# Kernel tuning notes

Measured on AMD Instinct MI355X. Metric: run time of the kernel, lower is better.

The kernel has to match this reference:

```python
import jax, jax.numpy as jnp
import numpy as np

H = 4096      # hidden_size
D = 1024      # mem_dim
A = 512       # attn_dim
B, LQ, TM = 4, 2048, 1500
EPS = 1e-5


def _layernorm(x, w, b):
    mu = jnp.mean(x, axis=-1, keepdims=True)
    var = jnp.var(x, axis=-1, keepdims=True)
    return (x - mu) * jax.lax.rsqrt(var + EPS) * w + b


def setup_inputs() -> dict:
    key = jax.random.key(0)
    ks = jax.random.split(key, 12)
    s = lambda fan_in: 1.0 / np.sqrt(fan_in)
    return {
        "hidden": jax.random.normal(ks[0], (B, LQ, H), jnp.float32),
        "mem": jax.random.normal(ks[1], (B, TM, D), jnp.float32),
        "mem_mask": jnp.zeros((B, TM), dtype=bool),
        "Wq": jax.random.uniform(ks[2], (H, A), jnp.float32, -s(H), s(H)),
        "bq": jnp.zeros((A,), jnp.float32),
        "Wk": jax.random.uniform(ks[3], (D, A), jnp.float32, -s(D), s(D)),
        "bk": jnp.zeros((A,), jnp.float32),
        "Wv": jax.random.uniform(ks[4], (D, A), jnp.float32, -s(D), s(D)),
        "bv": jnp.zeros((A,), jnp.float32),
        "Wo": jax.random.uniform(ks[5], (A, H), jnp.float32, -s(A), s(A)),
        "bo": jnp.zeros((H,), jnp.float32),
        "ln_in_w": jnp.ones((H,), jnp.float32),
        "ln_in_b": jnp.zeros((H,), jnp.float32),
        "ln_out_w": jnp.ones((H,), jnp.float32),
        "ln_out_b": jnp.zeros((H,), jnp.float32),
        "gate_logit": jnp.float32(-2.0),
    }


def reference(hidden, mem, mem_mask, Wq, bq, Wk, bk, Wv, bv, Wo, bo,
              ln_in_w, ln_in_b, ln_out_w, ln_out_b, gate_logit):
    h_norm = _layernorm(hidden, ln_in_w, ln_in_b)            # [B,LQ,H]
    Q = h_norm @ Wq + bq                                     # [B,LQ,A]
    K = mem @ Wk + bk                                        # [B,TM,A]
    V = mem @ Wv + bv                                        # [B,TM,A]
    scale = 1.0 / jnp.sqrt(jnp.float32(Q.shape[-1]))
    scores = jnp.einsum('bqa,bka->bqk', Q, K) * scale        # [B,LQ,TM]
    scores = jnp.where(mem_mask[:, None, :], jnp.float32(-1e30), scores)
    attn = jax.nn.softmax(scores, axis=-1)
    context = jnp.einsum('bqk,bka->bqa', attn, V)            # [B,LQ,A]
    context_h = context @ Wo + bo                            # [B,LQ,H]
    out_base = _layernorm(hidden + context_h, ln_out_w, ln_out_b)
    g = jax.nn.sigmoid(gate_logit)
    return hidden + g * (out_base - hidden)
```

## Files before the change

### kernel.cpp

```cpp
#include <hip/hip_runtime.h>
#include <cstdint>
#include <cstddef>

#define H_   4096
#define D_   1024
#define A_   512
#define B_   4
#define LQ_  2048
#define TM_  1500
#define TMP_ 1536
#define EPS_ 1e-5f

typedef __attribute__((ext_vector_type(8))) _Float16 half8;
typedef __attribute__((ext_vector_type(4))) _Float16 half4v;
typedef __attribute__((ext_vector_type(4))) float f32x4;

__device__ __forceinline__ void gload_lds16(void* g, void* l) {
  __builtin_amdgcn_global_load_lds((__attribute__((address_space(1))) void*)g,
                                   (__attribute__((address_space(3))) void*)l,
                                   16, 0, 0);
}

template <int OUTMODE>
__device__ __forceinline__ void gemm_tile(
    const _Float16* __restrict__ A, int lda,
    const _Float16* __restrict__ Bt, int ldb,
    const float* __restrict__ bias,
    void* __restrict__ C, int ldc,
    int Mvalid, int m0, int n0, int kbase, int kiters, float scale,
    _Float16* As, _Float16* Bs,
    const unsigned char* __restrict__ mrow, float* __restrict__ lsum, int nvalid) {
  const int tid = threadIdx.x;
  const int lane = tid & 63;
  const int wave = tid >> 6;

  f32x4 acc[4][4];
#pragma unroll
  for (int i = 0; i < 4; ++i)
#pragma unroll
    for (int jj = 0; jj < 4; ++jj) acc[i][jj] = (f32x4){0.f, 0.f, 0.f, 0.f};

  const _Float16* gA[2];
  const _Float16* gB[2];
  _Float16* lA[2];
  _Float16* lB[2];
#pragma unroll
  for (int i = 0; i < 2; ++i) {
    const int c = wave * 64 + lane + 256 * i;
    const int r = c >> 2;
    const int cs = c & 3;
    const int col = (cs ^ ((r >> 1) & 3)) * 8;
    int ra = m0 + r;
    if (ra >= Mvalid) ra = Mvalid - 1;
    gA[i] = A + (size_t)ra * lda + kbase + col;
    gB[i] = Bt + (size_t)(n0 + r) * ldb + kbase + col;
    lA[i] = As + wave * 512 + i * 2048;
    lB[i] = Bs + wave * 512 + i * 2048;
  }

  const int wm = (wave >> 1) * 64;
  const int wn = (wave & 1) * 64;
  const int rsub = lane & 15;
  const int j = lane >> 4;
  const int slot = j ^ ((rsub >> 1) & 3);

  for (int kt = 0; kt < kiters; ++kt) {
    const int ko = kt * 32;
#pragma unroll
    for (int i = 0; i < 2; ++i) {
      gload_lds16((void*)(gA[i] + ko), (void*)lA[i]);
      gload_lds16((void*)(gB[i] + ko), (void*)lB[i]);
    }
    __syncthreads();
    half8 af[4], bfr[4];
#pragma unroll
    for (int x = 0; x < 4; ++x) {
      af[x]  = *(const half8*)&As[(wm + x * 16 + rsub) * 32 + slot * 8];
      bfr[x] = *(const half8*)&Bs[(wn + x * 16 + rsub) * 32 + slot * 8];
    }
#pragma unroll
    for (int mi = 0; mi < 4; ++mi)
#pragma unroll
      for (int ni = 0; ni < 4; ++ni)
        acc[mi][ni] = __builtin_amdgcn_mfma_f32_16x16x32_f16(af[mi], bfr[ni], acc[mi][ni], 0, 0, 0);
    __syncthreads();
  }

  const int cn = n0 + wn + rsub;
  const int rm = m0 + wm + j * 4;

  if (OUTMODE == 3) {
    bool ok[4];
#pragma unroll
    for (int ni = 0; ni < 4; ++ni) {
      const int n = cn + ni * 16;
      const int nc = n < nvalid ? n : nvalid - 1;
      ok[ni] = (n < nvalid) && (mrow[nc] == 0);
    }
#pragma unroll
    for (int mi = 0; mi < 4; ++mi) {
#pragma unroll
      for (int r = 0; r < 4; ++r) {
        const int m = rm + mi * 16 + r;
        float rowsum = 0.f;
#pragma unroll
        for (int ni = 0; ni < 4; ++ni) {
          const int n = cn + ni * 16;
          const float e = ok[ni] ? __expf(acc[mi][ni][r] * scale) : 0.f;
          ((_Float16*)C)[(size_t)m * ldc + n] = (_Float16)e;
          rowsum += e;
        }
#pragma unroll
        for (int d = 1; d < 16; d <<= 1) rowsum += __shfl_xor(rowsum, d);
        if (rsub == 0) atomicAdd(&lsum[m], rowsum);
      }
    }
    return;
  }

  if (OUTMODE == 1) {
#pragma unroll
    for (int ni = 0; ni < 4; ++ni) {
      const int n = cn + ni * 16;
      const float bi = bias ? bias[n] : 0.f;
#pragma unroll
      for (int mi = 0; mi < 4; ++mi) {
        half4v pk;
#pragma unroll
        for (int r = 0; r < 4; ++r) pk[r] = (_Float16)(acc[mi][ni][r] * scale + bi);
        *(half4v*)&((_Float16*)C)[(size_t)n * ldc + rm + mi * 16] = pk;
      }
    }
    return;
  }

#pragma unroll
  for (int ni = 0; ni < 4; ++ni) {
    const int n = cn + ni * 16;
    const float bi = (OUTMODE == 0 && bias) ? bias[n] : 0.f;
#pragma unroll
    for (int mi = 0; mi < 4; ++mi) {
#pragma unroll
      for (int r = 0; r < 4; ++r) {
        const int m = rm + mi * 16 + r;
        const float v = acc[mi][ni][r] * scale + bi;
        if (OUTMODE == 0) ((_Float16*)C)[(size_t)m * ldc + n] = (_Float16)v;
        else ((float*)C)[(size_t)m * ldc + n] = v;
      }
    }
  }
}

template <int OUTMODE>
__global__ __launch_bounds__(256) void gemm_nt_kernel(
    const _Float16* __restrict__ Aall, size_t strideA, int lda,
    const _Float16* __restrict__ Btall, size_t strideB, int ldb,
    const float* __restrict__ bias,
    void* __restrict__ Call, size_t strideC, size_t strideS,
    int ldc, int Mvalid, int kiters, int nslices, int sliceK, float scale) {
  __shared__ __align__(16) _Float16 As[4096];
  __shared__ __align__(16) _Float16 Bs[4096];
  const int z = blockIdx.z;
  const int batch = z / nslices;
  const int slice = z % nslices;
  const _Float16* A = Aall + (size_t)batch * strideA;
  const _Float16* Bt = Btall + (size_t)batch * strideB;
  char* C = (char*)Call + ((size_t)batch * strideC + (size_t)slice * strideS) *
                          (OUTMODE == 2 ? 4 : 2);
  gemm_tile<OUTMODE>(A, lda, Bt, ldb, bias, (void*)C, ldc, Mvalid,
                     blockIdx.y * 128, blockIdx.x * 128, slice * sliceK, kiters,
                     scale, As, Bs, nullptr, nullptr, 0);
}

__global__ __launch_bounds__(256) void scores_kernel(
    const _Float16* __restrict__ Qh, const _Float16* __restrict__ Kp,
    _Float16* __restrict__ sc, const unsigned char* __restrict__ mask,
    float* __restrict__ lsum) {
  __shared__ __align__(16) _Float16 As[4096];
  __shared__ __align__(16) _Float16 Bs[4096];
  const int b = blockIdx.z;
  gemm_tile<3>(Qh + (size_t)b * LQ_ * A_, A_, Kp + (size_t)b * TMP_ * A_, A_, nullptr,
               (void*)(sc + (size_t)b * LQ_ * TMP_), TMP_, LQ_,
               blockIdx.y * 128, blockIdx.x * 128, 0, 16, 0.044194173824159216f,
               As, Bs, mask + (size_t)b * TM_, lsum + (size_t)b * LQ_, TM_);
}

__global__ __launch_bounds__(256) void qkv_kernel(
    const _Float16* __restrict__ hnorm, const _Float16* __restrict__ WqT,
    float* __restrict__ Qpart,
    const _Float16* __restrict__ memh, const _Float16* __restrict__ WkT,
    const float* __restrict__ bk, _Float16* __restrict__ Kp,
    const _Float16* __restrict__ WvT, const float* __restrict__ bv,
    _Float16* __restrict__ VT) {
  __shared__ __align__(16) _Float16 As[4096];
  __shared__ __align__(16) _Float16 Bs[4096];
  const int bid = blockIdx.x;
  if (bid < 512) {
    const int nb = bid & 3, mb = (bid >> 2) & 63, ks = bid >> 8;
    gemm_tile<2>(hnorm, H_, WqT, H_, nullptr,
                 (void*)(Qpart + (size_t)ks * 8192 * A_), A_,
                 8192, mb * 128, nb * 128, ks * 2048, 64, 1.f, As, Bs,
                 nullptr, nullptr, 0);
  } else if (bid < 704) {
    const int t = bid - 512;
    const int nb = t & 3, mb = (t >> 2) % 12, b = t / 48;
    gemm_tile<0>(memh + (size_t)b * TM_ * D_, D_, WkT, D_, bk,
                 (void*)(Kp + (size_t)b * TMP_ * A_), A_,
                 TM_, mb * 128, nb * 128, 0, 32, 1.f, As, Bs,
                 nullptr, nullptr, 0);
  } else {
    const int t = bid - 704;
    const int nb = t & 3, mb = (t >> 2) % 12, b = t / 48;
    gemm_tile<1>(memh + (size_t)b * TM_ * D_, D_, WvT, D_, bv,
                 (void*)(VT + (size_t)b * A_ * TMP_), TMP_,
                 TM_, mb * 128, nb * 128, 0, 32, 1.f, As, Bs,
                 nullptr, nullptr, 0);
  }
}

__global__ __launch_bounds__(256) void qreduce_kernel(
    const float* __restrict__ p, const float* __restrict__ bias,
    _Float16* __restrict__ out, float* __restrict__ lsum) {
  const int bid = blockIdx.x;
  if (bid >= 4096) {
    lsum[(bid - 4096) * 256 + threadIdx.x] = 0.f;
    return;
  }
  const size_t i = ((size_t)bid * 256 + threadIdx.x) * 4;
  const float4 a = *(const float4*)(p + i);
  const float4 b = *(const float4*)(p + (size_t)8192 * A_ + i);
  const float4 bi = *(const float4*)(bias + (i & (A_ - 1)));
  half4v o;
  o.x = (_Float16)(a.x + b.x + bi.x);
  o.y = (_Float16)(a.y + b.y + bi.y);
  o.z = (_Float16)(a.z + b.z + bi.z);
  o.w = (_Float16)(a.w + b.w + bi.w);
  *(half4v*)(out + i) = o;
}

__global__ __launch_bounds__(256) void areduce_kernel(
    const float* __restrict__ p, const float* __restrict__ lsum,
    _Float16* __restrict__ out) {
  const size_t S = (size_t)B_ * LQ_ * A_;
  const size_t i = ((size_t)blockIdx.x * 256 + threadIdx.x) * 4;
  const float4 a = *(const float4*)(p + i);
  const float4 b = *(const float4*)(p + S + i);
  const float4 c = *(const float4*)(p + 2 * S + i);
  const float inv = 1.f / lsum[i >> 9];
  half4v o;
  o.x = (_Float16)((a.x + b.x + c.x) * inv);
  o.y = (_Float16)((a.y + b.y + c.y) * inv);
  o.z = (_Float16)((a.z + b.z + c.z) * inv);
  o.w = (_Float16)((a.w + b.w + c.w) * inv);
  *(half4v*)(out + i) = o;
}

__global__ __launch_bounds__(256) void prep_kernel(
    const float* __restrict__ hidden, const float* __restrict__ lnw,
    const float* __restrict__ lnb, _Float16* __restrict__ hnorm,
    const float* __restrict__ mem, _Float16* __restrict__ memh,
    const float* __restrict__ Wq, _Float16* __restrict__ WqT,
    const float* __restrict__ Wk, _Float16* __restrict__ WkT,
    const float* __restrict__ Wv, _Float16* __restrict__ WvT,
    const float* __restrict__ Wo, _Float16* __restrict__ WoT) {
  __shared__ float smem[32 * 33];
  int bid = blockIdx.x;
  const int t = threadIdx.x;
  if (bid < 8192) {
    const float* x = hidden + (size_t)bid * H_;
    _Float16* y = hnorm + (size_t)bid * H_;
    float4 v[4];
    float s = 0.f, ss = 0.f;
#pragma unroll
    for (int i = 0; i < 4; ++i) {
      v[i] = ((const float4*)x)[t + 256 * i];
      s  += v[i].x + v[i].y + v[i].z + v[i].w;
      ss += v[i].x * v[i].x + v[i].y * v[i].y + v[i].z * v[i].z + v[i].w * v[i].w;
    }
    const int lane = t & 63, wv = t >> 6;
#pragma unroll
    for (int off = 32; off; off >>= 1) { s += __shfl_down(s, off); ss += __shfl_down(ss, off); }
    if (lane == 0) { smem[wv] = s; smem[4 + wv] = ss; }
    __syncthreads();
    s  = smem[0] + smem[1] + smem[2] + smem[3];
    ss = smem[4] + smem[5] + smem[6] + smem[7];
    const float mu = s * (1.f / H_);
    const float var = ss * (1.f / H_) - mu * mu;
    const float rstd = rsqrtf(var + EPS_);
#pragma unroll
    for (int i = 0; i < 4; ++i) {
      float4 wv4 = ((const float4*)lnw)[t + 256 * i];
      float4 bv4 = ((const float4*)lnb)[t + 256 * i];
      half4v o;
      o.x = (_Float16)((v[i].x - mu) * rstd * wv4.x + bv4.x);
      o.y = (_Float16)((v[i].y - mu) * rstd * wv4.y + bv4.y);
      o.z = (_Float16)((v[i].z - mu) * rstd * wv4.z + bv4.z);
      o.w = (_Float16)((v[i].w - mu) * rstd * wv4.w + bv4.w);
      ((half4v*)y)[t + 256 * i] = o;
    }
    return;
  }
  bid -= 8192;
  if (bid < 1500) {
    const size_t i = ((size_t)bid * 256 + t) * 4;
    float4 f = *(const float4*)(mem + i);
    half4v o;
    o.x = (_Float16)f.x; o.y = (_Float16)f.y; o.z = (_Float16)f.z; o.w = (_Float16)f.w;
    *(half4v*)(memh + i) = o;
    return;
  }
  bid -= 1500;
  const float* src;
  _Float16* dst;
  int R, C;
  if (bid < 2048) { src = Wq; dst = WqT; R = 4096; C = 512; }
  else if (bid < 2048 + 512) { bid -= 2048; src = Wk; dst = WkT; R = 1024; C = 512; }
  else if (bid < 2048 + 1024) { bid -= 2048 + 512; src = Wv; dst = WvT; R = 1024; C = 512; }
  else { bid -= 2048 + 1024; src = Wo; dst = WoT; R = 512; C = 4096; }
  const int nbx = C / 32;
  const int bx = bid % nbx, by = bid / nbx;
  const int tx = t & 31, ty = t >> 5;
  const int c0 = bx * 32, r0 = by * 32;
#pragma unroll
  for (int i = 0; i < 32; i += 8)
    smem[(ty + i) * 33 + tx] = src[(size_t)(r0 + ty + i) * C + c0 + tx];
  __syncthreads();
#pragma unroll
  for (int i = 0; i < 32; i += 8)
    dst[(size_t)(c0 + ty + i) * R + r0 + tx] = (_Float16)smem[tx * 33 + ty + i];
}

__global__ __launch_bounds__(256) void ln2_gate_kernel(
    const float* __restrict__ hidden_, const _Float16* __restrict__ ctxh_,
    const float* __restrict__ w, const float* __restrict__ bvec,
    const float* __restrict__ gate_logit, float* __restrict__ out_) {
  const int row = blockIdx.x;
  const float* h = hidden_ + (size_t)row * H_;
  const _Float16* c = ctxh_ + (size_t)row * H_;
  float* o = out_ + (size_t)row * H_;
  const int t = threadIdx.x;
  float4 hv[4];
  float xv[16];
  float s = 0.f, ss = 0.f;
#pragma unroll
  for (int i = 0; i < 4; ++i) {
    hv[i] = ((const float4*)h)[t + 256 * i];
    half4v cv = ((const half4v*)c)[t + 256 * i];
    xv[4 * i + 0] = hv[i].x + (float)cv.x;
    xv[4 * i + 1] = hv[i].y + (float)cv.y;
    xv[4 * i + 2] = hv[i].z + (float)cv.z;
    xv[4 * i + 3] = hv[i].w + (float)cv.w;
    s  += xv[4 * i + 0] + xv[4 * i + 1] + xv[4 * i + 2] + xv[4 * i + 3];
    ss += xv[4 * i + 0] * xv[4 * i + 0] + xv[4 * i + 1] * xv[4 * i + 1] +
          xv[4 * i + 2] * xv[4 * i + 2] + xv[4 * i + 3] * xv[4 * i + 3];
  }
  __shared__ float red[2][4];
  const int lane = t & 63, wv = t >> 6;
#pragma unroll
  for (int off = 32; off; off >>= 1) { s += __shfl_down(s, off); ss += __shfl_down(ss, off); }
  if (lane == 0) { red[0][wv] = s; red[1][wv] = ss; }
  __syncthreads();
  s  = red[0][0] + red[0][1] + red[0][2] + red[0][3];
  ss = red[1][0] + red[1][1] + red[1][2] + red[1][3];
  const float mu = s * (1.f / H_);
  const float var = ss * (1.f / H_) - mu * mu;
  const float rstd = rsqrtf(var + EPS_);
  const float g = 1.f / (1.f + __expf(-gate_logit[0]));
#pragma unroll
  for (int i = 0; i < 4; ++i) {
    float4 wv4 = ((const float4*)w)[t + 256 * i];
    float4 bv4 = ((const float4*)bvec)[t + 256 * i];
    float4 ov;
    ov.x = hv[i].x + g * ((xv[4 * i + 0] - mu) * rstd * wv4.x + bv4.x - hv[i].x);
    ov.y = hv[i].y + g * ((xv[4 * i + 1] - mu) * rstd * wv4.y + bv4.y - hv[i].y);
    ov.z = hv[i].z + g * ((xv[4 * i + 2] - mu) * rstd * wv4.z + bv4.z - hv[i].z);
    ov.w = hv[i].w + g * ((xv[4 * i + 3] - mu) * rstd * wv4.w + bv4.w - hv[i].w);
    ((float4*)o)[t + 256 * i] = ov;
  }
}

extern "C" void kernel_launch(void* const* d_in, const int* in_sizes, int n_in,
                              void* d_out, int out_size, void* d_ws, size_t ws_size,
                              hipStream_t stream) {
  const float* hidden = (const float*)d_in[0];
  const float* mem    = (const float*)d_in[1];
  const unsigned char* mask = (const unsigned char*)d_in[2];
  const float* Wq = (const float*)d_in[3];
  const float* bq = (const float*)d_in[4];
  const float* Wk = (const float*)d_in[5];
  const float* bk = (const float*)d_in[6];
  const float* Wv = (const float*)d_in[7];
  const float* bv = (const float*)d_in[8];
  const float* Wo = (const float*)d_in[9];
  const float* bo = (const float*)d_in[10];
  const float* lnw1 = (const float*)d_in[11];
  const float* lnb1 = (const float*)d_in[12];
  const float* lnw2 = (const float*)d_in[13];
  const float* lnb2 = (const float*)d_in[14];
  const float* gate = (const float*)d_in[15];
  float* out = (float*)d_out;

  _Float16* p = (_Float16*)d_ws;
  _Float16* hnorm = p; p += (size_t)8192 * H_;
  _Float16* Qh    = p; p += (size_t)8192 * A_;
  _Float16* memh  = p; p += (size_t)6000 * D_;
  _Float16* WqT   = p; p += (size_t)A_ * H_;
  _Float16* WkT   = p; p += (size_t)A_ * D_;
  _Float16* WvT   = p; p += (size_t)A_ * D_;
  _Float16* WoT   = p; p += (size_t)H_ * A_;
  _Float16* Kp    = p; p += (size_t)B_ * TMP_ * A_;
  _Float16* VT    = p; p += (size_t)B_ * A_ * TMP_;
  _Float16* sc    = p; p += (size_t)B_ * LQ_ * TMP_;
  _Float16* ctx   = p; p += (size_t)8192 * A_;
  float* Qpart = (float*)sc;
  float* Apart = (float*)hnorm;
  float* lsum  = (float*)WkT;

  prep_kernel<<<8192 + 1500 + 2048 + 512 + 512 + 2048, 256, 0, stream>>>(
      hidden, lnw1, lnb1, hnorm, mem, memh, Wq, WqT, Wk, WkT, Wv, WvT, Wo, WoT);
  qkv_kernel<<<896, 256, 0, stream>>>(hnorm, WqT, Qpart, memh, WkT, bk, Kp, WvT, bv, VT);
  qreduce_kernel<<<4096 + 32, 256, 0, stream>>>(Qpart, bq, Qh, lsum);
  scores_kernel<<<dim3(12, 16, 4), 256, 0, stream>>>(Qh, Kp, sc, mask, lsum);
  gemm_nt_kernel<2><<<dim3(4, 16, 12), 256, 0, stream>>>(
      sc, (size_t)LQ_ * TMP_, TMP_, VT, (size_t)A_ * TMP_, TMP_, nullptr,
      (void*)Apart, (size_t)LQ_ * A_, (size_t)B_ * LQ_ * A_, A_, LQ_, 16, 3, 512, 1.f);
  areduce_kernel<<<4096, 256, 0, stream>>>(Apart, lsum, ctx);
  gemm_nt_kernel<0><<<dim3(32, 64, 1), 256, 0, stream>>>(
      ctx, 0, A_, WoT, 0, A_, bo, (void*)hnorm, 0, 0, H_, 8192, 16, 1, 0, 1.f);
  ln2_gate_kernel<<<8192, 256, 0, stream>>>(hidden, hnorm, lnw2, lnb2, gate, out);
}
```

Before: 524.9 us.

## Double-buffer LDS tiles in GEMM and remap block IDs across XCDs

The GEMM tile loop now uses two LDS buffers, issuing the global-to-LDS load for the next K step while MFMAs run on the current one. This halves the barriers per K step and hides load latency. Block IDs are also permuted so that consecutive tiles land on the same XCD (id&7 striding), aiming for better L2 reuse on MI355X. It doubles LDS per block (32KB), which may reduce occupancy. The loop assumes kiters is even, and the swizzle assumes the block count divides by 8.

Measured after the change: 537.1 us. 1.02x slower.

```diff
diff --git a/kernel.cpp b/kernel.cpp
--- a/kernel.cpp
+++ b/kernel.cpp
@@ -64,26 +64,39 @@
   const int j = lane >> 4;
   const int slot = j ^ ((rsub >> 1) & 3);
 
-  for (int kt = 0; kt < kiters; ++kt) {
+  auto stage = [&](int buf, int kt) {
     const int ko = kt * 32;
 #pragma unroll
     for (int i = 0; i < 2; ++i) {
-      gload_lds16((void*)(gA[i] + ko), (void*)lA[i]);
-      gload_lds16((void*)(gB[i] + ko), (void*)lB[i]);
-    }
-    __syncthreads();
+      gload_lds16((void*)(gA[i] + ko), (void*)(lA[i] + buf * 4096));
+      gload_lds16((void*)(gB[i] + ko), (void*)(lB[i] + buf * 4096));
+    }
+  };
+  auto compute = [&](int buf) {
+    const _Float16* Ab = As + buf * 4096;
+    const _Float16* Bb = Bs + buf * 4096;
     half8 af[4], bfr[4];
 #pragma unroll
     for (int x = 0; x < 4; ++x) {
-      af[x]  = *(const half8*)&As[(wm + x * 16 + rsub) * 32 + slot * 8];
-      bfr[x] = *(const half8*)&Bs[(wn + x * 16 + rsub) * 32 + slot * 8];
+      af[x]  = *(const half8*)&Ab[(wm + x * 16 + rsub) * 32 + slot * 8];
+      bfr[x] = *(const half8*)&Bb[(wn + x * 16 + rsub) * 32 + slot * 8];
     }
 #pragma unroll
     for (int mi = 0; mi < 4; ++mi)
 #pragma unroll
       for (int ni = 0; ni < 4; ++ni)
         acc[mi][ni] = __builtin_amdgcn_mfma_f32_16x16x32_f16(af[mi], bfr[ni], acc[mi][ni], 0, 0, 0);
+  };
+
+  stage(0, 0);
+  __syncthreads();
+  for (int kt = 0; kt < kiters; kt += 2) {
+    stage(1, kt + 1);
+    compute(0);
     __syncthreads();
+    if (kt + 2 < kiters) stage(0, kt + 2);
+    compute(1);
+    if (kt + 2 < kiters) __syncthreads();
   }
 
   const int cn = n0 + wn + rsub;
@@ -158,17 +171,23 @@
     const float* __restrict__ bias,
     void* __restrict__ Call, size_t strideC, size_t strideS,
     int ldc, int Mvalid, int kiters, int nslices, int sliceK, float scale) {
-  __shared__ __align__(16) _Float16 As[4096];
-  __shared__ __align__(16) _Float16 Bs[4096];
-  const int z = blockIdx.z;
-  const int batch = z / nslices;
-  const int slice = z % nslices;
+  __shared__ __align__(16) _Float16 As[8192];
+  __shared__ __align__(16) _Float16 Bs[8192];
+  const int nx = gridDim.x, ny = gridDim.y;
+  int id = (int)blockIdx.x + nx * ((int)blockIdx.y + ny * (int)blockIdx.z);
+  const int tot = nx * ny * (int)gridDim.z;
+  id = (id & 7) * (tot >> 3) + (id >> 3);
+  const int bx = id % nx;
+  const int by = (id / nx) % ny;
+  const int bz = id / (nx * ny);
+  const int batch = bz / nslices;
+  const int slice = bz % nslices;
   const _Float16* A = Aall + (size_t)batch * strideA;
   const _Float16* Bt = Btall + (size_t)batch * strideB;
   char* C = (char*)Call + ((size_t)batch * strideC + (size_t)slice * strideS) *
                           (OUTMODE == 2 ? 4 : 2);
   gemm_tile<OUTMODE>(A, lda, Bt, ldb, bias, (void*)C, ldc, Mvalid,
-                     blockIdx.y * 128, blockIdx.x * 128, slice * sliceK, kiters,
+                     by * 128, bx * 128, slice * sliceK, kiters,
                      scale, As, Bs, nullptr, nullptr, 0);
 }
 
@@ -176,12 +195,18 @@
     const _Float16* __restrict__ Qh, const _Float16* __restrict__ Kp,
     _Float16* __restrict__ sc, const unsigned char* __restrict__ mask,
     float* __restrict__ lsum) {
-  __shared__ __align__(16) _Float16 As[4096];
-  __shared__ __align__(16) _Float16 Bs[4096];
-  const int b = blockIdx.z;
+  __shared__ __align__(16) _Float16 As[8192];
+  __shared__ __align__(16) _Float16 Bs[8192];
+  const int nx = gridDim.x, ny = gridDim.y;
+  int id = (int)blockIdx.x + nx * ((int)blockIdx.y + ny * (int)blockIdx.z);
+  const int tot = nx * ny * (int)gridDim.z;
+  id = (id & 7) * (tot >> 3) + (id >> 3);
+  const int bx = id % nx;
+  const int by = (id / nx) % ny;
+  const int b = id / (nx * ny);
   gemm_tile<3>(Qh + (size_t)b * LQ_ * A_, A_, Kp + (size_t)b * TMP_ * A_, A_, nullptr,
                (void*)(sc + (size_t)b * LQ_ * TMP_), TMP_, LQ_,
-               blockIdx.y * 128, blockIdx.x * 128, 0, 16, 0.044194173824159216f,
+               by * 128, bx * 128, 0, 16, 0.044194173824159216f,
                As, Bs, mask + (size_t)b * TM_, lsum + (size_t)b * LQ_, TM_);
 }
 
@@ -192,24 +217,27 @@
     const float* __restrict__ bk, _Float16* __restrict__ Kp,
     const _Float16* __restrict__ WvT, const float* __restrict__ bv,
     _Float16* __restrict__ VT) {
-  __shared__ __align__(16) _Float16 As[4096];
-  __shared__ __align__(16) _Float16 Bs[4096];
-  const int bid = blockIdx.x;
-  if (bid < 512) {
+  __shared__ __align__(16) _Float16 As[8192];
+  __shared__ __align__(16) _Float16 Bs[8192];
+  const int bid0 = blockIdx.x;
+  if (bid0 < 512) {
+    const int bid = ((bid0 & 7) << 6) | (bid0 >> 3);
     const int nb = bid & 3, mb = (bid >> 2) & 63, ks = bid >> 8;
     gemm_tile<2>(hnorm, H_, WqT, H_, nullptr,
                  (void*)(Qpart + (size_t)ks * 8192 * A_), A_,
                  8192, mb * 128, nb * 128, ks * 2048, 64, 1.f, As, Bs,
                  nullptr, nullptr, 0);
-  } else if (bid < 704) {
-    const int t = bid - 512;
+  } else if (bid0 < 704) {
+    int t = bid0 - 512;
+    t = (t & 7) * 24 + (t >> 3);
     const int nb = t & 3, mb = (t >> 2) % 12, b = t / 48;
     gemm_tile<0>(memh + (size_t)b * TM_ * D_, D_, WkT, D_, bk,
                  (void*)(Kp + (size_t)b * TMP_ * A_), A_,
                  TM_, mb * 128, nb * 128, 0, 32, 1.f, As, Bs,
                  nullptr, nullptr, 0);
   } else {
-    const int t = bid - 704;
+    int t = bid0 - 704;
+    t = (t & 7) * 24 + (t >> 3);
     const int nb = t & 3, mb = (t >> 2) % 12, b = t / 48;
     gemm_tile<1>(memh + (size_t)b * TM_ * D_, D_, WvT, D_, bv,
                  (void*)(VT + (size_t)b * A_ * TMP_), TMP_,
```
